# Optimization experiments

Measured on AMD Instinct MI355X. Metric: run time of the kernel, lower is better.

## Reference

```python
import jax, jax.numpy as jnp
import numpy as np

EMBED = 256
HEADS = 8
GROUP = 64
HEAD_DIM = EMBED // HEADS
N = 131072

def setup_inputs() -> dict:
    key = jax.random.key(0)
    k1, k2, k3 = jax.random.split(key, 3)
    s_in = 1.0 / np.sqrt(EMBED)
    x = jax.random.normal(k1, (N, EMBED), dtype=jnp.float32)
    w_qkv = jax.random.normal(k2, (3 * EMBED, EMBED), dtype=jnp.float32) * s_in  # nn.Linear weight [out,in]
    w_out = jax.random.normal(k3, (EMBED, EMBED), dtype=jnp.float32) * s_in
    b_out = jnp.zeros((EMBED,), dtype=jnp.float32)
    return {"x": x, "w_qkv": w_qkv, "w_out": w_out, "b_out": b_out}

def reference(x, w_qkv, w_out, b_out):
    Ntok, C = x.shape
    ng = Ntok // GROUP  # number of groups
    qkv = x @ w_qkv.T                      # (N, 3C)
    qkv = qkv.reshape(Ntok, 3, C)
    q, k, v = qkv[:, 0], qkv[:, 1], qkv[:, 2]

    def to_heads(t):
        # '(n g) (h c) -> (n h) g c'
        t = t.reshape(ng, GROUP, HEADS, HEAD_DIM)
        return t.transpose(0, 2, 1, 3).reshape(ng * HEADS, GROUP, HEAD_DIM)

    q, k, v = to_heads(q), to_heads(k), to_heads(v)
    # grouped attention over local windows of size GROUP
    energy = jnp.einsum('nqd,nkd->nqk', q, k)           # (n*h, g, g)
    attn = jax.nn.softmax(energy / jnp.sqrt(jnp.float32(C)), axis=-1)  # scale by sqrt(embed_size), as in source
    out = jnp.einsum('nql,nld->nqd', attn, v)           # (n*h, g, hd)
    # '(n h) g c -> (n g) (h c)'
    out = out.reshape(ng, HEADS, GROUP, HEAD_DIM).transpose(0, 2, 1, 3).reshape(Ntok, C)
    return out @ w_out.T + b_out
```

## Files before the change

kernel.cpp:

```cpp
#include <hip/hip_runtime.h>
#include <stdint.h>

typedef __attribute__((ext_vector_type(8))) short s16x8;
typedef __attribute__((ext_vector_type(4))) float f32x4;

__device__ __forceinline__ unsigned short f32_bf16(float f) {
  union { float f; uint32_t u; } v; v.f = f;
  return (unsigned short)((v.u + 0x7FFFu + ((v.u >> 16) & 1u)) >> 16);
}

__global__ void convert_w(const float* __restrict__ wqkv,
                          const float* __restrict__ wout,
                          unsigned short* __restrict__ o) {
  int i = blockIdx.x * 256 + threadIdx.x;
  if (i < 768 * 256) o[i] = f32_bf16(wqkv[i]);
  else               o[i] = f32_bf16(wout[i - 768 * 256]);
}

__global__ __launch_bounds__(512) void qkv_attn(
    const float* __restrict__ x,
    const unsigned short* __restrict__ wqkv,
    unsigned short* __restrict__ aout) {
  __shared__ unsigned short xt[64 * 256];
  __shared__ unsigned short wb[8][6144];

  const int g    = blockIdx.x;
  const int tid  = threadIdx.x;
  const int w    = tid >> 6;
  const int lane = tid & 63;
  const int l15  = lane & 15;
  const int l4   = lane >> 4;

  {
    const int row = tid >> 3;
    const int c0  = (tid & 7) * 32;
    const float* src = x + (size_t)(g * 64 + row) * 256 + c0;
#pragma unroll
    for (int c = 0; c < 32; c += 8) {
      float4 f0 = *(const float4*)(src + c);
      float4 f1 = *(const float4*)(src + c + 4);
      uint32_t p0 = f32_bf16(f0.x) | ((uint32_t)f32_bf16(f0.y) << 16);
      uint32_t p1 = f32_bf16(f0.z) | ((uint32_t)f32_bf16(f0.w) << 16);
      uint32_t p2 = f32_bf16(f1.x) | ((uint32_t)f32_bf16(f1.y) << 16);
      uint32_t p3 = f32_bf16(f1.z) | ((uint32_t)f32_bf16(f1.w) << 16);
      uint32_t byte = (uint32_t)(row * 512 + (c0 + c) * 2);
      byte ^= (row & 7) << 4;
      *(uint4*)((char*)xt + byte) = make_uint4(p0, p1, p2, p3);
    }
  }
  __syncthreads();

  f32x4 acc[6][4];
#pragma unroll
  for (int t = 0; t < 6; ++t)
#pragma unroll
    for (int m = 0; m < 4; ++m) acc[t][m] = (f32x4){0.f, 0.f, 0.f, 0.f};

  for (int kk = 0; kk < 8; ++kk) {
    s16x8 a[4];
#pragma unroll
    for (int m = 0; m < 4; ++m) {
      int row = 16 * m + l15;
      uint32_t byte = (uint32_t)(row * 512 + kk * 64 + l4 * 16) ^ ((row & 7) << 4);
      a[m] = *(const s16x8*)((const char*)xt + byte);
    }
#pragma unroll
    for (int t = 0; t < 6; ++t) {
      int wrow = (t >> 1) * 256 + w * 32 + (t & 1) * 16 + l15;
      s16x8 b = *(const s16x8*)(wqkv + (size_t)wrow * 256 + kk * 32 + l4 * 8);
#pragma unroll
      for (int m = 0; m < 4; ++m)
        acc[t][m] = __builtin_amdgcn_mfma_f32_16x16x32_bf16(a[m], b, acc[t][m], 0, 0, 0);
    }
  }

  unsigned short* q_l = wb[w];
  unsigned short* k_l = wb[w] + 2048;
  unsigned short* vt  = wb[w] + 4096;

#pragma unroll
  for (int t = 0; t < 4; ++t) {
    unsigned short* dst = (t < 2) ? q_l : k_l;
    int col = (t & 1) * 16 + l15;
#pragma unroll
    for (int m = 0; m < 4; ++m) {
#pragma unroll
      for (int r = 0; r < 4; ++r) {
        int row = 16 * m + l4 * 4 + r;
        uint32_t byte = (uint32_t)(row * 64 + col * 2) ^ ((row & 3) << 4);
        *(unsigned short*)((char*)dst + byte) = f32_bf16(acc[t][m][r]);
      }
    }
  }
#pragma unroll
  for (int t = 4; t < 6; ++t) {
    int d = (t - 4) * 16 + l15;
#pragma unroll
    for (int m = 0; m < 4; ++m) {
      uint32_t p0 = f32_bf16(acc[t][m][0]) | ((uint32_t)f32_bf16(acc[t][m][1]) << 16);
      uint32_t p1 = f32_bf16(acc[t][m][2]) | ((uint32_t)f32_bf16(acc[t][m][3]) << 16);
      uint32_t byte = (uint32_t)(d * 128 + m * 32 + l4 * 8) ^ ((d & 7) << 4);
      *(uint2*)((char*)vt + byte) = make_uint2(p0, p1);
    }
  }

  f32x4 e[4][4];
#pragma unroll
  for (int m = 0; m < 4; ++m)
#pragma unroll
    for (int n = 0; n < 4; ++n) e[m][n] = (f32x4){0.f, 0.f, 0.f, 0.f};

  {
    s16x8 qa[4], kb[4];
#pragma unroll
    for (int m = 0; m < 4; ++m) {
      int row = 16 * m + l15;
      uint32_t byte = (uint32_t)(row * 64 + l4 * 16) ^ ((row & 3) << 4);
      qa[m] = *(const s16x8*)((const char*)q_l + byte);
      kb[m] = *(const s16x8*)((const char*)k_l + byte);
    }
#pragma unroll
    for (int m = 0; m < 4; ++m)
#pragma unroll
      for (int n = 0; n < 4; ++n)
        e[m][n] = __builtin_amdgcn_mfma_f32_16x16x32_bf16(qa[m], kb[n], e[m][n], 0, 0, 0);
  }

  const float s = 0.0625f;
  unsigned short* P = wb[w];
#pragma unroll
  for (int m = 0; m < 4; ++m) {
#pragma unroll
    for (int r = 0; r < 4; ++r) {
      float mx = fmaxf(fmaxf(e[m][0][r], e[m][1][r]), fmaxf(e[m][2][r], e[m][3][r]));
#pragma unroll
      for (int d = 1; d < 16; d <<= 1) mx = fmaxf(mx, __shfl_xor(mx, d));
      float p0 = __expf((e[m][0][r] - mx) * s);
      float p1 = __expf((e[m][1][r] - mx) * s);
      float p2 = __expf((e[m][2][r] - mx) * s);
      float p3 = __expf((e[m][3][r] - mx) * s);
      float sum = p0 + p1 + p2 + p3;
#pragma unroll
      for (int d = 1; d < 16; d <<= 1) sum += __shfl_xor(sum, d);
      float rs = 1.0f / sum;
      int row = 16 * m + l4 * 4 + r;
      uint32_t rb = (uint32_t)(row * 128);
      uint32_t sw = (row & 7) << 4;
      *(unsigned short*)((char*)P + ((rb + (uint32_t)(l15 * 2))        ^ sw)) = f32_bf16(p0 * rs);
      *(unsigned short*)((char*)P + ((rb + (uint32_t)((16 + l15) * 2)) ^ sw)) = f32_bf16(p1 * rs);
      *(unsigned short*)((char*)P + ((rb + (uint32_t)((32 + l15) * 2)) ^ sw)) = f32_bf16(p2 * rs);
      *(unsigned short*)((char*)P + ((rb + (uint32_t)((48 + l15) * 2)) ^ sw)) = f32_bf16(p3 * rs);
    }
  }

  f32x4 o[4][2];
#pragma unroll
  for (int m = 0; m < 4; ++m) { o[m][0] = (f32x4){0.f,0.f,0.f,0.f}; o[m][1] = (f32x4){0.f,0.f,0.f,0.f}; }
#pragma unroll
  for (int kk2 = 0; kk2 < 2; ++kk2) {
    s16x8 pa[4], vb[2];
#pragma unroll
    for (int m = 0; m < 4; ++m) {
      int row = 16 * m + l15;
      uint32_t byte = (uint32_t)(row * 128 + kk2 * 64 + l4 * 16) ^ ((row & 7) << 4);
      pa[m] = *(const s16x8*)((const char*)P + byte);
    }
#pragma unroll
    for (int n = 0; n < 2; ++n) {
      int d = 16 * n + l15;
      uint32_t byte = (uint32_t)(d * 128 + kk2 * 64 + l4 * 16) ^ ((d & 7) << 4);
      vb[n] = *(const s16x8*)((const char*)vt + byte);
    }
#pragma unroll
    for (int m = 0; m < 4; ++m)
#pragma unroll
      for (int n = 0; n < 2; ++n)
        o[m][n] = __builtin_amdgcn_mfma_f32_16x16x32_bf16(pa[m], vb[n], o[m][n], 0, 0, 0);
  }

  unsigned short* dstbase = aout + (size_t)g * 64 * 256 + w * 32;
#pragma unroll
  for (int m = 0; m < 4; ++m)
#pragma unroll
    for (int n = 0; n < 2; ++n)
#pragma unroll
      for (int r = 0; r < 4; ++r) {
        int tok = 16 * m + l4 * 4 + r;
        dstbase[(size_t)tok * 256 + 16 * n + l15] = f32_bf16(o[m][n][r]);
      }
}

__global__ __launch_bounds__(256) void proj(
    const unsigned short* __restrict__ A,
    const unsigned short* __restrict__ Bw,
    const float* __restrict__ bias,
    float* __restrict__ out) {
  __shared__ unsigned short As[128 * 64];
  __shared__ unsigned short Bs[128 * 64];
  const int bm = blockIdx.x, bn = blockIdx.y;
  const int tid = threadIdx.x;
  const int w = tid >> 6, lane = tid & 63;
  const int l15 = lane & 15, l4 = lane >> 4;
  const int wr = w >> 1, wc = w & 1;

  f32x4 acc[4][4];
#pragma unroll
  for (int mi = 0; mi < 4; ++mi)
#pragma unroll
    for (int ni = 0; ni < 4; ++ni) acc[mi][ni] = (f32x4){0.f, 0.f, 0.f, 0.f};

  const int srow = tid >> 1;
  const int sc0  = (tid & 1) * 32;
  const unsigned short* ga = A  + (size_t)(bm * 128 + srow) * 256 + sc0;
  const unsigned short* gb = Bw + (size_t)(bn * 128 + srow) * 256 + sc0;

  for (int kk = 0; kk < 4; ++kk) {
#pragma unroll
    for (int c = 0; c < 32; c += 8) {
      uint4 va = *(const uint4*)(ga + kk * 64 + c);
      uint4 vb = *(const uint4*)(gb + kk * 64 + c);
      uint32_t byte = (uint32_t)(srow * 128 + (sc0 + c) * 2) ^ ((srow & 7) << 4);
      *(uint4*)((char*)As + byte) = va;
      *(uint4*)((char*)Bs + byte) = vb;
    }
    __syncthreads();
#pragma unroll
    for (int k2 = 0; k2 < 2; ++k2) {
      s16x8 af[4], bf[4];
#pragma unroll
      for (int mi = 0; mi < 4; ++mi) {
        int row = wr * 64 + 16 * mi + l15;
        uint32_t byte = (uint32_t)(row * 128 + k2 * 64 + l4 * 16) ^ ((row & 7) << 4);
        af[mi] = *(const s16x8*)((const char*)As + byte);
      }
#pragma unroll
      for (int ni = 0; ni < 4; ++ni) {
        int row = wc * 64 + 16 * ni + l15;
        uint32_t byte = (uint32_t)(row * 128 + k2 * 64 + l4 * 16) ^ ((row & 7) << 4);
        bf[ni] = *(const s16x8*)((const char*)Bs + byte);
      }
#pragma unroll
      for (int mi = 0; mi < 4; ++mi)
#pragma unroll
        for (int ni = 0; ni < 4; ++ni)
          acc[mi][ni] = __builtin_amdgcn_mfma_f32_16x16x32_bf16(af[mi], bf[ni], acc[mi][ni], 0, 0, 0);
    }
    __syncthreads();
  }

#pragma unroll
  for (int mi = 0; mi < 4; ++mi)
#pragma unroll
    for (int ni = 0; ni < 4; ++ni) {
      int col = bn * 128 + wc * 64 + 16 * ni + l15;
      float b = bias[col];
#pragma unroll
      for (int r = 0; r < 4; ++r) {
        int row = bm * 128 + wr * 64 + 16 * mi + l4 * 4 + r;
        out[(size_t)row * 256 + col] = acc[mi][ni][r] + b;
      }
    }
}

extern "C" void kernel_launch(void* const* d_in, const int* in_sizes, int n_in,
                              void* d_out, int out_size, void* d_ws, size_t ws_size,
                              hipStream_t stream) {
  const float* x    = (const float*)d_in[0];
  const float* wqkv = (const float*)d_in[1];
  const float* wout = (const float*)d_in[2];
  const float* bout = (const float*)d_in[3];
  float* out = (float*)d_out;

  unsigned short* wq_bf = (unsigned short*)d_ws;
  unsigned short* wo_bf = wq_bf + 768 * 256;
  unsigned short* aout  = wo_bf + 256 * 256;

  convert_w<<<1024, 256, 0, stream>>>(wqkv, wout, wq_bf);
  qkv_attn<<<2048, 512, 0, stream>>>(x, wq_bf, aout);
  proj<<<dim3(1024, 2), 256, 0, stream>>>(aout, wo_bf, bout, out);
}
```

Before: 233.9 us.

## Keep Q/K/V in registers with cross-lane shuffles instead of per-wave LDS staging

The fused QKV+attention kernel drops the 96KB per-block LDS scratch for Q, K, V^T and P. It computes Q^T and K^T tiles (weights as the A operand), reshapes the MFMA accumulators into operand layouts with lane shuffles, runs the softmax along the column dimension in registers, and computes V in a second pass over the x tile. The smaller LDS footprint plus launch_bounds(512,4) should allow more blocks per CU and avoid LDS round trips. The cost is many extra shuffles, re-reading the x tile for V, and more register pressure.

After: 257.0 us. 1.1x slower.

```diff
diff --git a/kernel.cpp b/kernel.cpp
--- a/kernel.cpp
+++ b/kernel.cpp
@@ -1,4 +1,5 @@
 #include <hip/hip_runtime.h>
+#include <hip/hip_bf16.h>
 #include <stdint.h>
 
 typedef __attribute__((ext_vector_type(8))) short s16x8;
@@ -7,6 +8,26 @@
 __device__ __forceinline__ unsigned short f32_bf16(float f) {
   union { float f; uint32_t u; } v; v.f = f;
   return (unsigned short)((v.u + 0x7FFFu + ((v.u >> 16) & 1u)) >> 16);
+}
+
+__device__ __forceinline__ uint32_t pack_bf16(float lo, float hi) {
+  __hip_bfloat162 h = __float22bfloat162_rn(float2{lo, hi});
+  union { __hip_bfloat162 h; uint32_t u; } u; u.h = h; return u.u;
+}
+
+__device__ __forceinline__ s16x8 xchg(uint32_t lo0, uint32_t lo1,
+                                      uint32_t hi0, uint32_t hi1,
+                                      int srcA, int srcB, uint32_t hisel) {
+  int a0 = __shfl((int)lo0, srcA), b0 = __shfl((int)hi0, srcA);
+  int a1 = __shfl((int)lo1, srcA), b1 = __shfl((int)hi1, srcA);
+  int a2 = __shfl((int)lo0, srcB), b2 = __shfl((int)hi0, srcB);
+  int a3 = __shfl((int)lo1, srcB), b3 = __shfl((int)hi1, srcB);
+  union { uint32_t u[4]; s16x8 v; } r;
+  r.u[0] = hisel ? (uint32_t)b0 : (uint32_t)a0;
+  r.u[1] = hisel ? (uint32_t)b1 : (uint32_t)a1;
+  r.u[2] = hisel ? (uint32_t)b2 : (uint32_t)a2;
+  r.u[3] = hisel ? (uint32_t)b3 : (uint32_t)a3;
+  return r.v;
 }
 
 __global__ void convert_w(const float* __restrict__ wqkv,
@@ -17,16 +38,15 @@
   else               o[i] = f32_bf16(wout[i - 768 * 256]);
 }
 
-__global__ __launch_bounds__(512) void qkv_attn(
+__global__ __launch_bounds__(512, 4) void qkv_attn(
     const float* __restrict__ x,
     const unsigned short* __restrict__ wqkv,
     unsigned short* __restrict__ aout) {
   __shared__ unsigned short xt[64 * 256];
-  __shared__ unsigned short wb[8][6144];
 
   const int g    = blockIdx.x;
   const int tid  = threadIdx.x;
-  const int w    = tid >> 6;
+  const int h    = tid >> 6;
   const int lane = tid & 63;
   const int l15  = lane & 15;
   const int l4   = lane >> 4;
@@ -35,159 +55,172 @@
     const int row = tid >> 3;
     const int c0  = (tid & 7) * 32;
     const float* src = x + (size_t)(g * 64 + row) * 256 + c0;
+    const uint32_t swz = (uint32_t)(row & 7) << 4;
 #pragma unroll
     for (int c = 0; c < 32; c += 8) {
       float4 f0 = *(const float4*)(src + c);
       float4 f1 = *(const float4*)(src + c + 4);
-      uint32_t p0 = f32_bf16(f0.x) | ((uint32_t)f32_bf16(f0.y) << 16);
-      uint32_t p1 = f32_bf16(f0.z) | ((uint32_t)f32_bf16(f0.w) << 16);
-      uint32_t p2 = f32_bf16(f1.x) | ((uint32_t)f32_bf16(f1.y) << 16);
-      uint32_t p3 = f32_bf16(f1.z) | ((uint32_t)f32_bf16(f1.w) << 16);
-      uint32_t byte = (uint32_t)(row * 512 + (c0 + c) * 2);
-      byte ^= (row & 7) << 4;
+      uint32_t p0 = pack_bf16(f0.x, f0.y);
+      uint32_t p1 = pack_bf16(f0.z, f0.w);
+      uint32_t p2 = pack_bf16(f1.x, f1.y);
+      uint32_t p3 = pack_bf16(f1.z, f1.w);
+      uint32_t byte = ((uint32_t)(row * 512 + (c0 + c) * 2)) ^ swz;
       *(uint4*)((char*)xt + byte) = make_uint4(p0, p1, p2, p3);
     }
   }
   __syncthreads();
 
-  f32x4 acc[6][4];
-#pragma unroll
-  for (int t = 0; t < 6; ++t)
-#pragma unroll
-    for (int m = 0; m < 4; ++m) acc[t][m] = (f32x4){0.f, 0.f, 0.f, 0.f};
+  const uint32_t swz   = (uint32_t)(l15 & 7) << 4;
+  const int      srcA  = l15 + ((lane & 16) << 1);
+  const int      srcB  = srcA + 16;
+  const uint32_t hisel = (uint32_t)(lane & 32);
+
+  const unsigned short* wbase = wqkv + (size_t)(h * 32 + l15) * 256 + l4 * 8;
+
+  f32x4 qT[2][4], kT[2][4];
+#pragma unroll
+  for (int t = 0; t < 2; ++t)
+#pragma unroll
+    for (int m = 0; m < 4; ++m) {
+      qT[t][m] = (f32x4){0.f, 0.f, 0.f, 0.f};
+      kT[t][m] = (f32x4){0.f, 0.f, 0.f, 0.f};
+    }
 
   for (int kk = 0; kk < 8; ++kk) {
     s16x8 a[4];
 #pragma unroll
     for (int m = 0; m < 4; ++m) {
-      int row = 16 * m + l15;
-      uint32_t byte = (uint32_t)(row * 512 + kk * 64 + l4 * 16) ^ ((row & 7) << 4);
+      uint32_t byte = ((uint32_t)((16 * m + l15) * 512 + kk * 64 + l4 * 16)) ^ swz;
       a[m] = *(const s16x8*)((const char*)xt + byte);
     }
 #pragma unroll
-    for (int t = 0; t < 6; ++t) {
-      int wrow = (t >> 1) * 256 + w * 32 + (t & 1) * 16 + l15;
-      s16x8 b = *(const s16x8*)(wqkv + (size_t)wrow * 256 + kk * 32 + l4 * 8);
-#pragma unroll
-      for (int m = 0; m < 4; ++m)
-        acc[t][m] = __builtin_amdgcn_mfma_f32_16x16x32_bf16(a[m], b, acc[t][m], 0, 0, 0);
-    }
-  }
-
-  unsigned short* q_l = wb[w];
-  unsigned short* k_l = wb[w] + 2048;
-  unsigned short* vt  = wb[w] + 4096;
-
-#pragma unroll
-  for (int t = 0; t < 4; ++t) {
-    unsigned short* dst = (t < 2) ? q_l : k_l;
-    int col = (t & 1) * 16 + l15;
-#pragma unroll
-    for (int m = 0; m < 4; ++m) {
+    for (int t = 0; t < 2; ++t) {
+      const unsigned short* wp = wbase + (size_t)(16 * t) * 256 + kk * 32;
+      s16x8 wq = *(const s16x8*)(wp);
+      s16x8 wk = *(const s16x8*)(wp + 256 * 256);
+#pragma unroll
+      for (int m = 0; m < 4; ++m) {
+        qT[t][m] = __builtin_amdgcn_mfma_f32_16x16x32_bf16(wq, a[m], qT[t][m], 0, 0, 0);
+        kT[t][m] = __builtin_amdgcn_mfma_f32_16x16x32_bf16(wk, a[m], kT[t][m], 0, 0, 0);
+      }
+    }
+  }
+
+  s16x8 kA[4], qB[4];
+#pragma unroll
+  for (int m = 0; m < 4; ++m) {
+    uint32_t q00 = pack_bf16(qT[0][m][0], qT[0][m][1]);
+    uint32_t q01 = pack_bf16(qT[0][m][2], qT[0][m][3]);
+    uint32_t q10 = pack_bf16(qT[1][m][0], qT[1][m][1]);
+    uint32_t q11 = pack_bf16(qT[1][m][2], qT[1][m][3]);
+    qB[m] = xchg(q00, q01, q10, q11, srcA, srcB, hisel);
+    uint32_t k00 = pack_bf16(kT[0][m][0], kT[0][m][1]);
+    uint32_t k01 = pack_bf16(kT[0][m][2], kT[0][m][3]);
+    uint32_t k10 = pack_bf16(kT[1][m][0], kT[1][m][1]);
+    uint32_t k11 = pack_bf16(kT[1][m][2], kT[1][m][3]);
+    kA[m] = xchg(k00, k01, k10, k11, srcA, srcB, hisel);
+  }
+
+  f32x4 e[4][4];
+#pragma unroll
+  for (int m = 0; m < 4; ++m)
+#pragma unroll
+    for (int n = 0; n < 4; ++n) {
+      e[m][n] = (f32x4){0.f, 0.f, 0.f, 0.f};
+      e[m][n] = __builtin_amdgcn_mfma_f32_16x16x32_bf16(kA[m], qB[n], e[m][n], 0, 0, 0);
+    }
+
+  uint32_t pkP[4][4][2];
+#pragma unroll
+  for (int n = 0; n < 4; ++n) {
+    float mx = e[0][n][0];
+#pragma unroll
+    for (int m = 0; m < 4; ++m)
+#pragma unroll
+      for (int r = 0; r < 4; ++r) mx = fmaxf(mx, e[m][n][r]);
+    mx = fmaxf(mx, __shfl_xor(mx, 16));
+    mx = fmaxf(mx, __shfl_xor(mx, 32));
+    float p[4][4];
+    float sum = 0.f;
+#pragma unroll
+    for (int m = 0; m < 4; ++m)
 #pragma unroll
       for (int r = 0; r < 4; ++r) {
-        int row = 16 * m + l4 * 4 + r;
-        uint32_t byte = (uint32_t)(row * 64 + col * 2) ^ ((row & 3) << 4);
-        *(unsigned short*)((char*)dst + byte) = f32_bf16(acc[t][m][r]);
-      }
-    }
-  }
-#pragma unroll
-  for (int t = 4; t < 6; ++t) {
-    int d = (t - 4) * 16 + l15;
-#pragma unroll
-    for (int m = 0; m < 4; ++m) {
-      uint32_t p0 = f32_bf16(acc[t][m][0]) | ((uint32_t)f32_bf16(acc[t][m][1]) << 16);
-      uint32_t p1 = f32_bf16(acc[t][m][2]) | ((uint32_t)f32_bf16(acc[t][m][3]) << 16);
-      uint32_t byte = (uint32_t)(d * 128 + m * 32 + l4 * 8) ^ ((d & 7) << 4);
-      *(uint2*)((char*)vt + byte) = make_uint2(p0, p1);
-    }
-  }
-
-  f32x4 e[4][4];
-#pragma unroll
-  for (int m = 0; m < 4; ++m)
-#pragma unroll
-    for (int n = 0; n < 4; ++n) e[m][n] = (f32x4){0.f, 0.f, 0.f, 0.f};
-
-  {
-    s16x8 qa[4], kb[4];
-#pragma unroll
-    for (int m = 0; m < 4; ++m) {
-      int row = 16 * m + l15;
-      uint32_t byte = (uint32_t)(row * 64 + l4 * 16) ^ ((row & 3) << 4);
-      qa[m] = *(const s16x8*)((const char*)q_l + byte);
-      kb[m] = *(const s16x8*)((const char*)k_l + byte);
-    }
-#pragma unroll
-    for (int m = 0; m < 4; ++m)
-#pragma unroll
-      for (int n = 0; n < 4; ++n)
-        e[m][n] = __builtin_amdgcn_mfma_f32_16x16x32_bf16(qa[m], kb[n], e[m][n], 0, 0, 0);
-  }
-
-  const float s = 0.0625f;
-  unsigned short* P = wb[w];
+        float t = __expf((e[m][n][r] - mx) * 0.0625f);
+        p[m][r] = t;
+        sum += t;
+      }
+    sum += __shfl_xor(sum, 16);
+    sum += __shfl_xor(sum, 32);
+    float rs = 1.0f / sum;
+#pragma unroll
+    for (int m = 0; m < 4; ++m) {
+      pkP[n][m][0] = pack_bf16(p[m][0] * rs, p[m][1] * rs);
+      pkP[n][m][1] = pack_bf16(p[m][2] * rs, p[m][3] * rs);
+    }
+  }
+
+  f32x4 vv[4][2];
 #pragma unroll
   for (int m = 0; m < 4; ++m) {
-#pragma unroll
-    for (int r = 0; r < 4; ++r) {
-      float mx = fmaxf(fmaxf(e[m][0][r], e[m][1][r]), fmaxf(e[m][2][r], e[m][3][r]));
-#pragma unroll
-      for (int d = 1; d < 16; d <<= 1) mx = fmaxf(mx, __shfl_xor(mx, d));
-      float p0 = __expf((e[m][0][r] - mx) * s);
-      float p1 = __expf((e[m][1][r] - mx) * s);
-      float p2 = __expf((e[m][2][r] - mx) * s);
-      float p3 = __expf((e[m][3][r] - mx) * s);
-      float sum = p0 + p1 + p2 + p3;
-#pragma unroll
-      for (int d = 1; d < 16; d <<= 1) sum += __shfl_xor(sum, d);
-      float rs = 1.0f / sum;
-      int row = 16 * m + l4 * 4 + r;
-      uint32_t rb = (uint32_t)(row * 128);
-      uint32_t sw = (row & 7) << 4;
-      *(unsigned short*)((char*)P + ((rb + (uint32_t)(l15 * 2))        ^ sw)) = f32_bf16(p0 * rs);
-      *(unsigned short*)((char*)P + ((rb + (uint32_t)((16 + l15) * 2)) ^ sw)) = f32_bf16(p1 * rs);
-      *(unsigned short*)((char*)P + ((rb + (uint32_t)((32 + l15) * 2)) ^ sw)) = f32_bf16(p2 * rs);
-      *(unsigned short*)((char*)P + ((rb + (uint32_t)((48 + l15) * 2)) ^ sw)) = f32_bf16(p3 * rs);
-    }
-  }
+    vv[m][0] = (f32x4){0.f, 0.f, 0.f, 0.f};
+    vv[m][1] = (f32x4){0.f, 0.f, 0.f, 0.f};
+  }
+  for (int kk = 0; kk < 8; ++kk) {
+    s16x8 a[4];
+#pragma unroll
+    for (int m = 0; m < 4; ++m) {
+      uint32_t byte = ((uint32_t)((16 * m + l15) * 512 + kk * 64 + l4 * 16)) ^ swz;
+      a[m] = *(const s16x8*)((const char*)xt + byte);
+    }
+    const unsigned short* wp = wbase + (size_t)512 * 256 + kk * 32;
+    s16x8 wv0 = *(const s16x8*)(wp);
+    s16x8 wv1 = *(const s16x8*)(wp + 16 * 256);
+#pragma unroll
+    for (int m = 0; m < 4; ++m) {
+      vv[m][0] = __builtin_amdgcn_mfma_f32_16x16x32_bf16(a[m], wv0, vv[m][0], 0, 0, 0);
+      vv[m][1] = __builtin_amdgcn_mfma_f32_16x16x32_bf16(a[m], wv1, vv[m][1], 0, 0, 0);
+    }
+  }
+  uint32_t pkV[2][4][2];
+#pragma unroll
+  for (int t = 0; t < 2; ++t)
+#pragma unroll
+    for (int m = 0; m < 4; ++m) {
+      pkV[t][m][0] = pack_bf16(vv[m][t][0], vv[m][t][1]);
+      pkV[t][m][1] = pack_bf16(vv[m][t][2], vv[m][t][3]);
+    }
 
   f32x4 o[4][2];
 #pragma unroll
-  for (int m = 0; m < 4; ++m) { o[m][0] = (f32x4){0.f,0.f,0.f,0.f}; o[m][1] = (f32x4){0.f,0.f,0.f,0.f}; }
+  for (int nb = 0; nb < 4; ++nb) {
+    o[nb][0] = (f32x4){0.f, 0.f, 0.f, 0.f};
+    o[nb][1] = (f32x4){0.f, 0.f, 0.f, 0.f};
+  }
 #pragma unroll
   for (int kk2 = 0; kk2 < 2; ++kk2) {
-    s16x8 pa[4], vb[2];
-#pragma unroll
-    for (int m = 0; m < 4; ++m) {
-      int row = 16 * m + l15;
-      uint32_t byte = (uint32_t)(row * 128 + kk2 * 64 + l4 * 16) ^ ((row & 7) << 4);
-      pa[m] = *(const s16x8*)((const char*)P + byte);
-    }
-#pragma unroll
-    for (int n = 0; n < 2; ++n) {
-      int d = 16 * n + l15;
-      uint32_t byte = (uint32_t)(d * 128 + kk2 * 64 + l4 * 16) ^ ((d & 7) << 4);
-      vb[n] = *(const s16x8*)((const char*)vt + byte);
-    }
-#pragma unroll
-    for (int m = 0; m < 4; ++m)
-#pragma unroll
-      for (int n = 0; n < 2; ++n)
-        o[m][n] = __builtin_amdgcn_mfma_f32_16x16x32_bf16(pa[m], vb[n], o[m][n], 0, 0, 0);
-  }
-
-  unsigned short* dstbase = aout + (size_t)g * 64 * 256 + w * 32;
-#pragma unroll
-  for (int m = 0; m < 4; ++m)
-#pragma unroll
-    for (int n = 0; n < 2; ++n)
-#pragma unroll
-      for (int r = 0; r < 4; ++r) {
-        int tok = 16 * m + l4 * 4 + r;
-        dstbase[(size_t)tok * 256 + 16 * n + l15] = f32_bf16(o[m][n][r]);
-      }
+    s16x8 vB[2];
+#pragma unroll
+    for (int t = 0; t < 2; ++t)
+      vB[t] = xchg(pkV[t][2 * kk2][0], pkV[t][2 * kk2][1],
+                   pkV[t][2 * kk2 + 1][0], pkV[t][2 * kk2 + 1][1], srcA, srcB, hisel);
+#pragma unroll
+    for (int nb = 0; nb < 4; ++nb) {
+      s16x8 pA = xchg(pkP[nb][2 * kk2][0], pkP[nb][2 * kk2][1],
+                      pkP[nb][2 * kk2 + 1][0], pkP[nb][2 * kk2 + 1][1], srcA, srcB, hisel);
+      o[nb][0] = __builtin_amdgcn_mfma_f32_16x16x32_bf16(pA, vB[0], o[nb][0], 0, 0, 0);
+      o[nb][1] = __builtin_amdgcn_mfma_f32_16x16x32_bf16(pA, vB[1], o[nb][1], 0, 0, 0);
+    }
+  }
+
+  unsigned short* dst = aout + (size_t)g * 64 * 256 + h * 32;
+#pragma unroll
+  for (int nb = 0; nb < 4; ++nb)
+#pragma unroll
+    for (int t = 0; t < 2; ++t)
+#pragma unroll
+      for (int r = 0; r < 4; ++r)
+        dst[(size_t)(16 * nb + 4 * l4 + r) * 256 + 16 * t + l15] = f32_bf16(o[nb][t][r]);
 }
 
 __global__ __launch_bounds__(256) void proj(
```
